# Performance work log

Measured on AMD Instinct MI355X. Metric: run time of the kernel, lower is better.

The kernel has to match this reference:

```python
import jax, jax.numpy as jnp
import numpy as np

N_NODES = 50000
DEG = 32
HEADS = 4
OUT_F = 16
IN_F = 64
NEG_SLOPE = 0.01  # jax.nn.leaky_relu default


def setup_inputs() -> dict:
    key = jax.random.key(0)
    k_adj, k_mask, k_q, k_qw, k_kw, k_aw = jax.random.split(key, 6)
    adj = jax.random.randint(k_adj, (N_NODES, DEG), 0, N_NODES)
    pad = jax.random.uniform(k_mask, (N_NODES, DEG)) < 0.1
    adj = jnp.where(pad, -1, adj)
    Q = jax.random.normal(k_q, (IN_F, N_NODES), dtype=jnp.float32)
    qw_scale = 2 * np.sqrt(6.0 / (IN_F + OUT_F * HEADS))
    kw_scale = qw_scale
    a_scale = 2 * np.sqrt(6.0 / (OUT_F + HEADS))
    query_weight = (jax.random.uniform(k_qw, (HEADS, OUT_F, IN_F)) - 0.5) * qw_scale
    key_weight = (jax.random.uniform(k_kw, (HEADS, OUT_F, IN_F)) - 0.5) * kw_scale
    attn_weight = (jax.random.uniform(k_aw, (HEADS, OUT_F)) - 0.5) * a_scale
    return {
        'adj': adj,
        'Q': Q,
        'query_weight': query_weight.astype(jnp.float32),
        'key_weight': key_weight.astype(jnp.float32),
        'attn_weight': attn_weight.astype(jnp.float32),
    }


def reference(adj, Q, query_weight, key_weight, attn_weight):
    # K defaults to Q (self-attention over graph)
    K = Q
    # project keys: [H, O, N], then gather neighbors -> [H, O, N, deg]
    Ko = jnp.einsum('hoi,in->hon', key_weight, K)[..., adj]
    # project queries: [H, O, N]
    Qo = jnp.einsum('hoi,in->hon', query_weight, Q)
    # per-edge pre-activation and attention logits
    X = jax.nn.leaky_relu(Qo[..., None] + Ko, negative_slope=NEG_SLOPE)
    X = jnp.einsum('honk,ho->hnk', X, attn_weight)  # [H, N, deg]
    X = jnp.where(adj == -1, -jnp.inf, X)
    # rows with zero valid neighbors -> zero logits (uniform softmax, masked later)
    X = jnp.where((adj != -1).sum(-1, keepdims=True) == 0, 0.0, X)
    attn = jax.nn.softmax(X, axis=-1)
    # weighted aggregate of gathered keys -> [H, O, N]
    return jnp.einsum('hnk,honk->hon', jnp.where(adj == -1, 0.0, attn), Ko)
```

## Files before the change

kernel.cpp:

```cpp
#include <hip/hip_runtime.h>
#include <math.h>

#define DEG 32
#define NHO 64
#define NPW 4
#define NPB 16

typedef short  frag8  __attribute__((ext_vector_type(8)));
typedef float  f32x4  __attribute__((ext_vector_type(4)));

template <int CTRL>
__device__ __forceinline__ float dpp_add(float v) {
    int t = __builtin_amdgcn_update_dpp(0, __float_as_int(v), CTRL, 0xF, 0xF, true);
    return v + __int_as_float(t);
}

__device__ __forceinline__ unsigned bf16_rne(float f) {
    unsigned u = __float_as_uint(f);
    return (u + 0x7fffu + ((u >> 16) & 1u)) >> 16;
}

__global__ __launch_bounds__(256) void proj_mfma_kernel(
    const float* __restrict__ Q,
    const float* __restrict__ Wq,
    const float* __restrict__ Wk,
    unsigned short* __restrict__ Pqb,
    unsigned short* __restrict__ Pkb,
    int N)
{
    __shared__ unsigned qlds[64 * 33];
    __shared__ unsigned wlds[128 * 33];

    int t  = threadIdx.x;
    int n0 = blockIdx.x * 64;

    {
        int l    = t >> 1;
        int half = t & 1;
        const float* wr = (l < 64 ? Wq + (size_t)l * 64
                                  : Wk + (size_t)(l - 64) * 64) + half * 32;
#pragma unroll
        for (int r = 0; r < 16; r++) {
            float f0 = wr[2 * r], f1 = wr[2 * r + 1];
            wlds[l * 33 + half * 16 + r] = bf16_rne(f0) | (bf16_rne(f1) << 16);
        }
    }
    {
        int n  = t & 63;
        int gn = n0 + n;
        bool act = (gn < N);
#pragma unroll
        for (int r = 0; r < 8; r++) {
            int dp = (t >> 6) * 8 + r;
            int k  = dp * 2;
            float f0 = act ? Q[(size_t)k * N + gn] : 0.f;
            float f1 = act ? Q[(size_t)(k + 1) * N + gn] : 0.f;
            qlds[n * 33 + dp] = bf16_rne(f0) | (bf16_rne(f1) << 16);
        }
    }
    __syncthreads();

    int lane = t & 63;
    int w    = t >> 6;
    int li   = lane & 15;
    int quad = lane >> 4;

    f32x4 acc[8];
#pragma unroll
    for (int ot = 0; ot < 8; ot++) acc[ot] = (f32x4){0.f, 0.f, 0.f, 0.f};

#pragma unroll
    for (int ks = 0; ks < 2; ks++) {
        union { unsigned u[4]; frag8 f; } A;
        int abase = (w * 16 + li) * 33 + ks * 16 + quad * 4;
#pragma unroll
        for (int c = 0; c < 4; c++) A.u[c] = qlds[abase + c];
#pragma unroll
        for (int ot = 0; ot < 8; ot++) {
            union { unsigned u[4]; frag8 f; } B;
            int bbase = (ot * 16 + li) * 33 + ks * 16 + quad * 4;
#pragma unroll
            for (int c = 0; c < 4; c++) B.u[c] = wlds[bbase + c];
            acc[ot] = __builtin_amdgcn_mfma_f32_16x16x32_bf16(A.f, B.f, acc[ot],
                                                              0, 0, 0);
        }
    }

#pragma unroll
    for (int ot = 0; ot < 8; ot++) {
#pragma unroll
        for (int r = 0; r < 4; r++) {
            int node = n0 + w * 16 + quad * 4 + r;
            if (node < N) {
                unsigned short v = (unsigned short)bf16_rne(acc[ot][r]);
                if (ot < 4)
                    Pqb[(size_t)node * NHO + ot * 16 + li] = v;
                else
                    Pkb[(size_t)node * NHO + (ot - 4) * 16 + li] = v;
            }
        }
    }
}


__device__ __forceinline__ float swz_x16(float v) {
    return __int_as_float(__builtin_amdgcn_ds_swizzle(__float_as_int(v), 0x401F));
}
__device__ __forceinline__ float bprm(int addr, float v) {
    return __int_as_float(__builtin_amdgcn_ds_bpermute(addr, __float_as_int(v)));
}

__device__ __forceinline__ void gat_gather(uint2 (&dst)[8],
                                           const int4 lo, const int4 hi,
                                           const uint2* __restrict__ Pk64,
                                           int sl) {
    dst[0] = Pk64[(size_t)(lo.x < 0 ? 0 : lo.x) * 16 + sl];
    dst[1] = Pk64[(size_t)(lo.y < 0 ? 0 : lo.y) * 16 + sl];
    dst[2] = Pk64[(size_t)(lo.z < 0 ? 0 : lo.z) * 16 + sl];
    dst[3] = Pk64[(size_t)(lo.w < 0 ? 0 : lo.w) * 16 + sl];
    dst[4] = Pk64[(size_t)(hi.x < 0 ? 0 : hi.x) * 16 + sl];
    dst[5] = Pk64[(size_t)(hi.y < 0 ? 0 : hi.y) * 16 + sl];
    dst[6] = Pk64[(size_t)(hi.z < 0 ? 0 : hi.z) * 16 + sl];
    dst[7] = Pk64[(size_t)(hi.w < 0 ? 0 : hi.w) * 16 + sl];
}

__device__ __forceinline__ void gat_compute(
    const uint2 (&kv)[8], const int4 lo, const int4 hi, uint2 qraw,
    float c1_0, float c1_1, float c1_2, float c1_3,
    float c2_0, float c2_1, float c2_2, float c2_3,
    int slot, int sl, int bprm_x32, int col,
    float (&tile)[NHO][NPB + 1])
{
    float qp0 = __uint_as_float(qraw.x << 16);
    float qp1 = __uint_as_float(qraw.x & 0xffff0000u);
    float qp2 = __uint_as_float(qraw.y << 16);
    float qp3 = __uint_as_float(qraw.y & 0xffff0000u);

    float c1q = c1_0 * qp0;
    c1q = fmaf(c1_1, qp1, c1q);
    c1q = fmaf(c1_2, qp2, c1q);
    c1q = fmaf(c1_3, qp3, c1q);

    const int jt[8] = {lo.x, lo.y, lo.z, lo.w, hi.x, hi.y, hi.z, hi.w};

    float s = 0.f, a0 = 0.f, a1 = 0.f, a2 = 0.f, a3 = 0.f;
#pragma unroll
    for (int t = 0; t < 8; t++) {
        float kv0 = __uint_as_float(kv[t].x << 16);
        float kv1 = __uint_as_float(kv[t].x & 0xffff0000u);
        float kv2 = __uint_as_float(kv[t].y << 16);
        float kv3 = __uint_as_float(kv[t].y & 0xffff0000u);
        float x0 = qp0 + kv0, x1 = qp1 + kv1;
        float x2 = qp2 + kv2, x3 = qp3 + kv3;
        float c = fmaf(c1_0, kv0, c1q);
        c = fmaf(c1_1, kv1, c);
        c = fmaf(c1_2, kv2, c);
        c = fmaf(c1_3, kv3, c);
        c = fmaf(c2_0, fabsf(x0), c);
        c = fmaf(c2_1, fabsf(x1), c);
        c = fmaf(c2_2, fabsf(x2), c);
        c = fmaf(c2_3, fabsf(x3), c);
        c = dpp_add<0xB1>(c);
        c = dpp_add<0x4E>(c);
        float p = __builtin_amdgcn_exp2f(c);
        p = (jt[t] >= 0) ? p : 0.f;
        s += p;
        a0 = fmaf(p, kv0, a0);
        a1 = fmaf(p, kv1, a1);
        a2 = fmaf(p, kv2, a2);
        a3 = fmaf(p, kv3, a3);
    }

    s  += swz_x16(s);
    a0 += swz_x16(a0);
    a1 += swz_x16(a1);
    a2 += swz_x16(a2);
    a3 += swz_x16(a3);
    s  += bprm(bprm_x32, s);
    a0 += bprm(bprm_x32, a0);
    a1 += bprm(bprm_x32, a1);
    a2 += bprm(bprm_x32, a2);
    a3 += bprm(bprm_x32, a3);

    float rs = (s > 0.f) ? __builtin_amdgcn_rcpf(s) : 0.f;
    if (slot == 0) {
        tile[4 * sl + 0][col] = a0 * rs;
        tile[4 * sl + 1][col] = a1 * rs;
        tile[4 * sl + 2][col] = a2 * rs;
        tile[4 * sl + 3][col] = a3 * rs;
    }
}

__global__ __launch_bounds__(256, 4) void gat_kernel(
    const int*            __restrict__ adj,
    const unsigned short* __restrict__ Pqb,
    const unsigned short* __restrict__ Pkb,
    const float*          __restrict__ aw,
    float*                __restrict__ out,
    int N)
{
    __shared__ float tile[NHO][NPB + 1];

    int l    = threadIdx.x & 63;
    int wv   = threadIdx.x >> 6;
    int sl   = l & 15;
    int slot = l >> 4;

    const uint2* Pk64 = (const uint2*)Pkb;
    const uint2* Pq64 = (const uint2*)Pqb;

    float4 awq = *(const float4*)(aw + 4 * sl);
    const float L2E = 1.44269504f;
    float c1_0 = 0.505f * L2E * awq.x, c2_0 = 0.495f * L2E * awq.x;
    float c1_1 = 0.505f * L2E * awq.y, c2_1 = 0.495f * L2E * awq.y;
    float c1_2 = 0.505f * L2E * awq.z, c2_2 = 0.495f * L2E * awq.z;
    float c1_3 = 0.505f * L2E * awq.w, c2_3 = 0.495f * L2E * awq.w;

    int bprm_x32 = (l ^ 32) * 4;
    int nbase = blockIdx.x * NPB + wv * NPW;

    if (nbase + NPW <= N) {
        int4  aLo[NPW], aHi[NPW];
        uint2 qr[NPW];
#pragma unroll
        for (int ni = 0; ni < NPW; ni++) {
            const int* ap = adj + (size_t)(nbase + ni) * DEG + slot * 8;
            aLo[ni] = *(const int4*)ap;
            aHi[ni] = *(const int4*)(ap + 4);
            qr[ni]  = Pq64[(size_t)(nbase + ni) * 16 + sl];
        }

        uint2 kvA[8], kvB[8];
        gat_gather(kvA, aLo[0], aHi[0], Pk64, sl);

#pragma unroll
        for (int ni = 0; ni < NPW; ni++) {
            int col = wv * NPW + ni;
            if ((ni & 1) == 0) {
                if (ni + 1 < NPW)
                    gat_gather(kvB, aLo[ni + 1], aHi[ni + 1], Pk64, sl);
                gat_compute(kvA, aLo[ni], aHi[ni], qr[ni],
                            c1_0, c1_1, c1_2, c1_3, c2_0, c2_1, c2_2, c2_3,
                            slot, sl, bprm_x32, col, tile);
            } else {
                if (ni + 1 < NPW)
                    gat_gather(kvA, aLo[ni + 1], aHi[ni + 1], Pk64, sl);
                gat_compute(kvB, aLo[ni], aHi[ni], qr[ni],
                            c1_0, c1_1, c1_2, c1_3, c2_0, c2_1, c2_2, c2_3,
                            slot, sl, bprm_x32, col, tile);
            }
        }
    } else {
        uint2 kvA[8];
#pragma unroll 1
        for (int ni = 0; ni < NPW; ni++) {
            int n = nbase + ni;
            if (n < N) {
                const int* ap = adj + (size_t)n * DEG + slot * 8;
                int4 lo = *(const int4*)ap;
                int4 hi = *(const int4*)(ap + 4);
                uint2 qraw = Pq64[(size_t)n * 16 + sl];
                gat_gather(kvA, lo, hi, Pk64, sl);
                gat_compute(kvA, lo, hi, qraw,
                            c1_0, c1_1, c1_2, c1_3, c2_0, c2_1, c2_2, c2_3,
                            slot, sl, bprm_x32, wv * NPW + ni, tile);
            }
        }
    }
    __syncthreads();

    int n0 = blockIdx.x * NPB;
    int lr = threadIdx.x >> 2;
    int c4 = threadIdx.x & 3;
    int nc = n0 + c4 * 4;
    float4 v = make_float4(tile[lr][c4 * 4 + 0], tile[lr][c4 * 4 + 1],
                           tile[lr][c4 * 4 + 2], tile[lr][c4 * 4 + 3]);
    if (nc + 3 < N) {
        *(float4*)(out + (size_t)lr * N + nc) = v;
    } else {
#pragma unroll
        for (int e = 0; e < 4; e++)
            if (nc + e < N) out[(size_t)lr * N + nc + e] = (&v.x)[e];
    }
}

extern "C" void kernel_launch(void* const* d_in, const int* in_sizes, int n_in,
                              void* d_out, int out_size, void* d_ws, size_t ws_size,
                              hipStream_t stream) {
    const int*   adj = (const int*)  d_in[0];
    const float* Q   = (const float*)d_in[1];
    const float* qw  = (const float*)d_in[2];
    const float* kw  = (const float*)d_in[3];
    const float* aw  = (const float*)d_in[4];
    float*       out = (float*)d_out;

    int N = in_sizes[0] / DEG;

    unsigned short* Pqb = (unsigned short*)d_ws;
    unsigned short* Pkb = Pqb + (size_t)N * NHO;

    proj_mfma_kernel<<<(N + 63) / 64, 256, 0, stream>>>(Q, qw, kw, Pqb, Pkb, N);

    gat_kernel<<<(N + NPB - 1) / NPB, 256, 0, stream>>>(adj, Pqb, Pkb, aw, out, N);
}
```

Before: 106.4 us.

## Trade gather double-buffering for higher occupancy with bitmask validity and index prefetch

Removes the double-buffered neighbor gather and the up-front loading of all four nodes' adjacency rows. Each node's adjacency and query are now prefetched one step ahead, and validity is packed into an 8-bit mask. The launch bound is raised from 4 to 8 blocks per SM to cut register pressure and raise occupancy, relying on more resident waves to hide gather latency. The risk is less memory-level parallelism within a wave, since each gather is now consumed right after it is issued.

```diff
diff --git a/kernel.cpp b/kernel.cpp
--- a/kernel.cpp
+++ b/kernel.cpp
@@ -124,8 +124,21 @@
     dst[7] = Pk64[(size_t)(hi.w < 0 ? 0 : hi.w) * 16 + sl];
 }
 
+__device__ __forceinline__ unsigned gat_vmask(const int4 lo, const int4 hi) {
+    unsigned vm = 0;
+    vm |= (lo.x >= 0) ? 1u   : 0u;
+    vm |= (lo.y >= 0) ? 2u   : 0u;
+    vm |= (lo.z >= 0) ? 4u   : 0u;
+    vm |= (lo.w >= 0) ? 8u   : 0u;
+    vm |= (hi.x >= 0) ? 16u  : 0u;
+    vm |= (hi.y >= 0) ? 32u  : 0u;
+    vm |= (hi.z >= 0) ? 64u  : 0u;
+    vm |= (hi.w >= 0) ? 128u : 0u;
+    return vm;
+}
+
 __device__ __forceinline__ void gat_compute(
-    const uint2 (&kv)[8], const int4 lo, const int4 hi, uint2 qraw,
+    const uint2 (&kv)[8], unsigned vm, uint2 qraw,
     float c1_0, float c1_1, float c1_2, float c1_3,
     float c2_0, float c2_1, float c2_2, float c2_3,
     int slot, int sl, int bprm_x32, int col,
@@ -140,8 +153,6 @@
     c1q = fmaf(c1_1, qp1, c1q);
     c1q = fmaf(c1_2, qp2, c1q);
     c1q = fmaf(c1_3, qp3, c1q);
-
-    const int jt[8] = {lo.x, lo.y, lo.z, lo.w, hi.x, hi.y, hi.z, hi.w};
 
     float s = 0.f, a0 = 0.f, a1 = 0.f, a2 = 0.f, a3 = 0.f;
 #pragma unroll
@@ -163,7 +174,7 @@
         c = dpp_add<0xB1>(c);
         c = dpp_add<0x4E>(c);
         float p = __builtin_amdgcn_exp2f(c);
-        p = (jt[t] >= 0) ? p : 0.f;
+        p = (vm & (1u << t)) ? p : 0.f;
         s += p;
         a0 = fmaf(p, kv0, a0);
         a1 = fmaf(p, kv1, a1);
@@ -191,7 +202,7 @@
     }
 }
 
-__global__ __launch_bounds__(256, 4) void gat_kernel(
+__global__ __launch_bounds__(256, 8) void gat_kernel(
     const int*            __restrict__ adj,
     const unsigned short* __restrict__ Pqb,
     const unsigned short* __restrict__ Pkb,
@@ -220,38 +231,28 @@
     int nbase = blockIdx.x * NPB + wv * NPW;
 
     if (nbase + NPW <= N) {
-        int4  aLo[NPW], aHi[NPW];
-        uint2 qr[NPW];
+        const int* ap0 = adj + (size_t)nbase * DEG + slot * 8;
+        int4  lo   = *(const int4*)ap0;
+        int4  hi   = *(const int4*)(ap0 + 4);
+        uint2 qraw = Pq64[(size_t)nbase * 16 + sl];
+
 #pragma unroll
         for (int ni = 0; ni < NPW; ni++) {
-            const int* ap = adj + (size_t)(nbase + ni) * DEG + slot * 8;
-            aLo[ni] = *(const int4*)ap;
-            aHi[ni] = *(const int4*)(ap + 4);
-            qr[ni]  = Pq64[(size_t)(nbase + ni) * 16 + sl];
-        }
-
-        uint2 kvA[8], kvB[8];
-        gat_gather(kvA, aLo[0], aHi[0], Pk64, sl);
-
-#pragma unroll
-        for (int ni = 0; ni < NPW; ni++) {
-            int col = wv * NPW + ni;
-            if ((ni & 1) == 0) {
-                if (ni + 1 < NPW)
-                    gat_gather(kvB, aLo[ni + 1], aHi[ni + 1], Pk64, sl);
-                gat_compute(kvA, aLo[ni], aHi[ni], qr[ni],
-                            c1_0, c1_1, c1_2, c1_3, c2_0, c2_1, c2_2, c2_3,
-                            slot, sl, bprm_x32, col, tile);
-            } else {
-                if (ni + 1 < NPW)
-                    gat_gather(kvA, aLo[ni + 1], aHi[ni + 1], Pk64, sl);
-                gat_compute(kvB, aLo[ni], aHi[ni], qr[ni],
-                            c1_0, c1_1, c1_2, c1_3, c2_0, c2_1, c2_2, c2_3,
-                            slot, sl, bprm_x32, col, tile);
+            uint2 kv[8];
+            gat_gather(kv, lo, hi, Pk64, sl);
+            unsigned vm  = gat_vmask(lo, hi);
+            uint2    cqr = qraw;
+            if (ni + 1 < NPW) {
+                const int* ap = adj + (size_t)(nbase + ni + 1) * DEG + slot * 8;
+                lo   = *(const int4*)ap;
+                hi   = *(const int4*)(ap + 4);
+                qraw = Pq64[(size_t)(nbase + ni + 1) * 16 + sl];
             }
+            gat_compute(kv, vm, cqr,
+                        c1_0, c1_1, c1_2, c1_3, c2_0, c2_1, c2_2, c2_3,
+                        slot, sl, bprm_x32, wv * NPW + ni, tile);
         }
     } else {
-        uint2 kvA[8];
 #pragma unroll 1
         for (int ni = 0; ni < NPW; ni++) {
             int n = nbase + ni;
@@ -260,8 +261,10 @@
                 int4 lo = *(const int4*)ap;
                 int4 hi = *(const int4*)(ap + 4);
                 uint2 qraw = Pq64[(size_t)n * 16 + sl];
-                gat_gather(kvA, lo, hi, Pk64, sl);
-                gat_compute(kvA, lo, hi, qraw,
+                uint2 kv[8];
+                gat_gather(kv, lo, hi, Pk64, sl);
+                unsigned vm = gat_vmask(lo, hi);
+                gat_compute(kv, vm, qraw,
                             c1_0, c1_1, c1_2, c1_3, c2_0, c2_1, c2_2, c2_3,
                             slot, sl, bprm_x32, wv * NPW + ni, tile);
             }
```

Measured after the change: 109.2 us. +2.6%, slower.
